# Performance work log

Measured on AMD Instinct MI355X. Metric: run time of the kernel, lower is better.

The kernel has to match this reference:

```python
import jax, jax.numpy as jnp
import numpy as np

TIME_SCALES = [1, 2, 4]
K = len(TIME_SCALES)      # 3 scales
N = 4                     # lcm(time_scales)
S = sum(TIME_SCALES)      # 7 slots
D_HEAD = 128              # d
D = S * D_HEAD            # 896
IO_DIM = 1024
RANK = 64
HIDDEN = 4 * D            # 3584
EPS = 1e-5


def _tables():
    active = np.empty((N, K), dtype=np.int64)
    perm = np.empty((N, K, N), dtype=np.int64)
    inv = np.empty((N, K, N), dtype=np.int64)
    ids = np.arange(N)
    for ph in range(N):
        off = 0
        for k, s in enumerate(TIME_SCALES):
            active[ph, k] = off + ph % s
            off += s
            j = ph % s
            alpha = N // s
            p = (ids + alpha * j) % N   # SHARED assignment
            perm[ph, k] = p
            ip = np.empty_like(p)
            ip[p] = ids
            inv[ph, k] = ip
    return active, perm, inv

ACTIVE, PERM, INV = _tables()


def _ln(x, scale, bias):
    mu = jnp.mean(x, axis=-1, keepdims=True)
    var = jnp.mean((x - mu) ** 2, axis=-1, keepdims=True)
    return (x - mu) * jax.lax.rsqrt(var + EPS) * scale + bias


def setup_inputs() -> dict:
    key = jax.random.key(0)
    ks = jax.random.split(key, 16)
    B, T = 8, 1024

    def w(k, shape, s=0.02):
        return jax.random.normal(k, shape, dtype=jnp.float32) * s

    return {
        "x": jax.random.normal(ks[0], (B, T, IO_DIM), dtype=jnp.float32),
        "enc_base_w": w(ks[1], (D, IO_DIM)),
        "enc_A_w": w(ks[2], (RANK, IO_DIM)),
        "enc_B": w(ks[3], (RANK, N, D)),
        "enc_beta": jnp.float32(0.01),
        "Wqkv": w(ks[4], (K, N, D_HEAD, 3 * D_HEAD)),
        "ln_attn_scale": jnp.ones((D_HEAD,), jnp.float32),
        "ln_attn_bias": jnp.zeros((D_HEAD,), jnp.float32),
        "ln_mixer_scale": jnp.ones((D,), jnp.float32),
        "ln_mixer_bias": jnp.zeros((D,), jnp.float32),
        "mixer_w1": w(ks[5], (HIDDEN, D)),
        "mixer_b1": jnp.zeros((HIDDEN,), jnp.float32),
        "mixer_w2": w(ks[6], (D, HIDDEN)),
        "mixer_b2": jnp.zeros((D,), jnp.float32),
        "dec_ln_scale": jnp.ones((N * D,), jnp.float32),
        "dec_ln_bias": jnp.zeros((N * D,), jnp.float32),
        "dec_down_w": w(ks[7], (RANK, N * D)),
        "dec_up_w": w(ks[8], (IO_DIM, RANK)),
        "phase": 1,
    }


def reference(x, enc_base_w, enc_A_w, enc_B, enc_beta, Wqkv,
              ln_attn_scale, ln_attn_bias, ln_mixer_scale, ln_mixer_bias,
              mixer_w1, mixer_b1, mixer_w2, mixer_b2,
              dec_ln_scale, dec_ln_bias, dec_down_w, dec_up_w, phase):
    B, T, _ = x.shape
    # ---- StreamLoRAEncoder: x [B,T,io] -> z0 [B,T,N,D]
    base = x @ enc_base_w.T                 # [B,T,D]
    h = x @ enc_A_w.T                       # [B,T,r]
    delta = jnp.einsum('btr,rnd->btnd', h, enc_B)
    z0 = base[:, :, None, :] + enc_beta * delta
    # ---- gather active slots for this phase (one slot per scale group)
    slots = ACTIVE[phase]                   # [K]
    z_slots = z0.reshape(B, T, N, S, D_HEAD)
    x_slot = z_slots[:, :, :, slots, :]     # [B,T,N,K,d]
    x_slot = _ln(x_slot, ln_attn_scale, ln_attn_bias)
    # ---- SHARED qkv projection (stream->head inverse perm, bmm, head->stream perm)
    x_in = x_slot.transpose(0, 1, 3, 2, 4)  # [B,T,K,N,d]
    kk = np.arange(K)[:, None]
    x_head = x_in[:, :, kk, INV[phase], :]  # [B,T,K,N,d]
    qkv = jnp.einsum('btknd,knde->btkne', x_head, Wqkv)  # [B,T,K,N,3d]
    qh, kh, vh = jnp.split(qkv, 3, axis=-1)
    p = PERM[phase]
    q = qh[:, :, kk, p, :].transpose(0, 3, 2, 1, 4).reshape(B, N * K, T, D_HEAD)
    k_ = kh[:, :, kk, p, :].transpose(0, 3, 2, 1, 4).reshape(B, N * K, T, D_HEAD)
    v = vh[:, :, kk, p, :].transpose(0, 3, 2, 1, 4).reshape(B, N * K, T, D_HEAD)
    # ---- causal attention over T per (stream, scale) head
    scores = jnp.einsum('bhtd,bhsd->bhts', q, k_) / np.float32(np.sqrt(D_HEAD))
    mask = jnp.tril(jnp.ones((T, T), dtype=bool))
    scores = jnp.where(mask, scores, jnp.float32(-1e9))
    attn = jax.nn.softmax(scores, axis=-1)
    out = jnp.einsum('bhts,bhsd->bhtd', attn, v)  # [B,N*K,T,d]
    # ---- scatter back to active slots (residual add)
    out5 = out.reshape(B, N, K, T, D_HEAD).transpose(0, 3, 1, 2, 4)  # [B,T,N,K,d]
    z1 = z_slots.at[:, :, :, slots, :].add(out5).reshape(B, T, N, D)
    # ---- mixer MLP (pre-LN residual)
    hm = _ln(z1, ln_mixer_scale, ln_mixer_bias)
    m = jax.nn.gelu(hm @ mixer_w1.T + mixer_b1, approximate=False) @ mixer_w2.T + mixer_b2
    z2 = z1 + m
    # ---- StreamLoRADecoder: concat streams, LN, rank-bottleneck projection
    cat = z2.reshape(B, T, N * D)
    y = _ln(cat, dec_ln_scale, dec_ln_bias) @ dec_down_w.T @ dec_up_w.T
    return y
```

## Files before the change

kernel.cpp:

```cpp
#include <hip/hip_runtime.h>
#include <hip/hip_bf16.h>
#include <math.h>


#define BT   8192
#define DH   128
#define DD   896
#define ND   3584
#define IO   1024
#define RK   64
#define HID  3584

typedef __attribute__((ext_vector_type(8))) short short8;
typedef __attribute__((ext_vector_type(4))) float f32x4;
typedef __hip_bfloat16 bf16;

#define DS_READ_B128(dst, p)                                                  \
    asm volatile("ds_read_b128 %0, %1"                                        \
                 : "=v"(dst)                                                  \
                 : "v"((const __attribute__((address_space(3))) bf16*)(p)))

__device__ __forceinline__ float gelu_f(float v)
{
    float u = v * 0.70710678118654752f;
    float a = fabsf(u);
    float t = __builtin_amdgcn_rcpf(1.0f + 0.3275911f * a);
    float p = t * (0.254829592f + t * (-0.284496736f + t * (1.421413741f +
              t * (-1.453152027f + t * 1.061405429f))));
    float er = 1.0f - p * __expf(-u * u);
    er = copysignf(er, u);
    return 0.5f * v * (1.0f + er);
}

template<int BM, int BN, int BK, int TM, int TN>
__global__ __launch_bounds__(256) void gemm_kernel(const float* __restrict__ A,
                                                   const float* __restrict__ B,
                                                   float* __restrict__ C,
                                                   int N, int Kd)
{
    constexpr int THREADS = (BM / TM) * (BN / TN);
    constexpr int LDA = BM + 4;
    constexpr int LDB = BN + 4;
    __shared__ float As[BK][LDA];
    __shared__ float Bs[BK][LDB];

    const int tid = threadIdx.x;
    constexpr int NX = BN / TN;
    const int tx = tid % NX;
    const int ty = tid / NX;
    const int row0 = blockIdx.y * BM;
    const int col0 = blockIdx.x * BN;

    float acc[TM][TN];
#pragma unroll
    for (int i = 0; i < TM; ++i)
#pragma unroll
        for (int j = 0; j < TN; ++j) acc[i][j] = 0.f;

    for (int k0 = 0; k0 < Kd; k0 += BK) {
        constexpr int AF4 = BM * BK / 4;
        for (int f = tid; f < AF4; f += THREADS) {
            int r  = f / (BK / 4);
            int c4 = (f % (BK / 4)) * 4;
            float4 v = *(const float4*)(A + (size_t)(row0 + r) * Kd + k0 + c4);
            As[c4 + 0][r] = v.x; As[c4 + 1][r] = v.y;
            As[c4 + 2][r] = v.z; As[c4 + 3][r] = v.w;
        }
        constexpr int BF4 = BN * BK / 4;
        for (int f = tid; f < BF4; f += THREADS) {
            int r  = f / (BK / 4);
            int c4 = (f % (BK / 4)) * 4;
            float4 v = *(const float4*)(B + (size_t)(col0 + r) * Kd + k0 + c4);
            Bs[c4 + 0][r] = v.x; Bs[c4 + 1][r] = v.y;
            Bs[c4 + 2][r] = v.z; Bs[c4 + 3][r] = v.w;
        }
        __syncthreads();

#pragma unroll
        for (int kk = 0; kk < BK; ++kk) {
            float a[TM], b[TN];
#pragma unroll
            for (int i = 0; i < TM; i += 4)
                *(float4*)&a[i] = *(const float4*)&As[kk][ty * TM + i];
#pragma unroll
            for (int j = 0; j < TN; j += 4)
                *(float4*)&b[j] = *(const float4*)&Bs[kk][tx * TN + j];
#pragma unroll
            for (int i = 0; i < TM; ++i)
#pragma unroll
                for (int j = 0; j < TN; ++j)
                    acc[i][j] = fmaf(a[i], b[j], acc[i][j]);
        }
        __syncthreads();
    }

    const int crow = row0 + ty * TM;
    const int ccol = col0 + tx * TN;
#pragma unroll
    for (int i = 0; i < TM; ++i) {
        float* cp = C + (size_t)(crow + i) * N + ccol;
#pragma unroll
        for (int j = 0; j < TN; ++j) cp[j] = acc[i][j];
    }
}

template<int BN, int EPI>
__global__ __launch_bounds__(512, 2) void gemm_bf16_256(
    const bf16* __restrict__ A,
    const bf16* __restrict__ B,
    float* __restrict__ Cf,
    bf16* __restrict__ Cb,
    int N, int Kd,
    const float* __restrict__ bias)
{
    constexpr int NR    = BN / 64;
    constexpr int WTN   = 16 * NR;
    constexpr int ASLOT = 256 * 32;
    constexpr int BSLOT = BN * 32;
    __shared__ bf16 As[4 * ASLOT];
    __shared__ bf16 Bs[4 * BSLOT];

    const int tid  = threadIdx.x;
    const int wave = tid >> 6;
    const int lane = tid & 63;
    const int wm = wave >> 2, wn = wave & 3;
    const int lr = lane & 15, lq = lane >> 4;

    const int gx  = gridDim.x;
    int fid = blockIdx.y * gx + blockIdx.x;
    const int cpx = (gx * gridDim.y) >> 3;
    fid = (fid & 7) * cpx + (fid >> 3);
    const int row0 = (fid / gx) * 256;
    const int col0 = (fid % gx) * BN;

    const int sr  = lane >> 2;
    const int scs = (((lane & 3) ^ ((lane >> 3) & 3)) << 3);
    const bf16* Ag = A + (size_t)(row0 + sr) * Kd + scs;
    const bf16* Bg = B + (size_t)(col0 + sr) * Kd + scs;

    const int scox = (lq * 8) ^ (((lr >> 1) & 3) << 3);

    f32x4 acc[8][NR];
#pragma unroll
    for (int i = 0; i < 8; ++i)
#pragma unroll
        for (int j = 0; j < NR; ++j) acc[i][j] = (f32x4){0.f, 0.f, 0.f, 0.f};

    const int NH = Kd >> 5;

    auto stage = [&](int h) {
        const int slot = h & 3;
#pragma unroll
        for (int i = 0; i < 2; ++i) {
            const int rg = (i * 8 + wave) * 16;
            __builtin_amdgcn_global_load_lds(
                (const __attribute__((address_space(1))) unsigned int*)
                    (Ag + (size_t)rg * Kd + h * 32),
                (__attribute__((address_space(3))) unsigned int*)
                    (As + slot * ASLOT + rg * 32),
                16, 0, 0);
        }
#pragma unroll
        for (int i = 0; i < BN / 128; ++i) {
            const int rg = (i * 8 + wave) * 16;
            __builtin_amdgcn_global_load_lds(
                (const __attribute__((address_space(1))) unsigned int*)
                    (Bg + (size_t)rg * Kd + h * 32),
                (__attribute__((address_space(3))) unsigned int*)
                    (Bs + slot * BSLOT + rg * 32),
                16, 0, 0);
        }
    };

    stage(0); stage(1); stage(2);

    for (int h = 0; h < NH; ++h) {
        if (h + 3 < NH) stage(h + 3);

        const int ahead = NH - 1 - h;
        if constexpr (BN == 256) {
            if (ahead >= 3)      asm volatile("s_waitcnt vmcnt(12)" ::: "memory");
            else if (ahead == 2) asm volatile("s_waitcnt vmcnt(8)"  ::: "memory");
            else if (ahead == 1) asm volatile("s_waitcnt vmcnt(4)"  ::: "memory");
            else                 asm volatile("s_waitcnt vmcnt(0)"  ::: "memory");
        } else {
            if (ahead >= 3)      asm volatile("s_waitcnt vmcnt(9)"  ::: "memory");
            else if (ahead == 2) asm volatile("s_waitcnt vmcnt(6)"  ::: "memory");
            else if (ahead == 1) asm volatile("s_waitcnt vmcnt(3)"  ::: "memory");
            else                 asm volatile("s_waitcnt vmcnt(0)"  ::: "memory");
        }
        __builtin_amdgcn_s_barrier();

        const bf16* Ab = As + (h & 3) * ASLOT;
        const bf16* Bb = Bs + (h & 3) * BSLOT;

        short8 bfr[NR], afr[8];
#pragma unroll
        for (int nt = 0; nt < NR; ++nt)
            DS_READ_B128(bfr[nt], Bb + (wn * WTN + nt * 16 + lr) * 32 + scox);
#pragma unroll
        for (int mt = 0; mt < 8; ++mt)
            DS_READ_B128(afr[mt], Ab + (wm * 128 + mt * 16 + lr) * 32 + scox);

        asm volatile("s_waitcnt lgkmcnt(0)" ::: "memory");
        __builtin_amdgcn_sched_barrier(0);

        __builtin_amdgcn_s_setprio(1);
#pragma unroll
        for (int mt = 0; mt < 8; ++mt)
#pragma unroll
            for (int nt = 0; nt < NR; ++nt)
                acc[mt][nt] = __builtin_amdgcn_mfma_f32_16x16x32_bf16(
                    afr[mt], bfr[nt], acc[mt][nt], 0, 0, 0);
        __builtin_amdgcn_s_setprio(0);

        __builtin_amdgcn_s_barrier();
    }

#pragma unroll
    for (int mt = 0; mt < 8; ++mt) {
#pragma unroll
        for (int nt = 0; nt < NR; ++nt) {
            const int col = col0 + wn * WTN + nt * 16 + lr;
            const bool cok = (col < N);
            const float bcol = (EPI == 0 || !cok) ? 0.f : bias[col];
#pragma unroll
            for (int r = 0; r < 4; ++r) {
                const int row = row0 + wm * 128 + mt * 16 + lq * 4 + r;
                float v = acc[mt][nt][r] + bcol;
                if (EPI == 1) {
                    if (cok) Cb[(size_t)row * N + col] = __float2bfloat16(gelu_f(v));
                } else if (EPI == 2) {
                    if (cok) Cf[(size_t)row * N + col] += v;
                } else {
                    if (cok) Cf[(size_t)row * N + col] = v;
                }
            }
        }
    }
}

__global__ __launch_bounds__(256) void pack_enc_kernel(const float* __restrict__ baseW,
                                                       const float* __restrict__ Aw,
                                                       const float* __restrict__ Bv,
                                                       const float* __restrict__ betap,
                                                       bf16* __restrict__ outp)
{
    __shared__ float Ps[64][68];
    __shared__ float Qs[64][68];
    const int tid = threadIdx.x;
    const int e0 = blockIdx.y * 64;
    const int k0 = blockIdx.x * 64;

    for (int f = tid; f < 1024; f += 256) {
        int r = f >> 4, c4 = (f & 15) << 2;
        *(float4*)&Ps[r][c4] = *(const float4*)(Bv + (size_t)r * ND + e0 + c4);
        *(float4*)&Qs[r][c4] = *(const float4*)(Aw + (size_t)r * IO + k0 + c4);
    }
    __syncthreads();

    const int tx = tid & 15, ty = tid >> 4;
    float acc[4][4];
#pragma unroll
    for (int i = 0; i < 4; ++i)
#pragma unroll
        for (int j = 0; j < 4; ++j) acc[i][j] = 0.f;

#pragma unroll 8
    for (int r = 0; r < 64; ++r) {
        float a[4], b[4];
        *(float4*)a = *(const float4*)&Ps[r][ty * 4];
        *(float4*)b = *(const float4*)&Qs[r][tx * 4];
#pragma unroll
        for (int i = 0; i < 4; ++i)
#pragma unroll
            for (int j = 0; j < 4; ++j) acc[i][j] = fmaf(a[i], b[j], acc[i][j]);
    }

    const float beta = betap[0];
#pragma unroll
    for (int i = 0; i < 4; ++i) {
        const int e = e0 + ty * 4 + i;
        const int d = e % DD;
#pragma unroll
        for (int j = 0; j < 4; ++j) {
            const int k = k0 + tx * 4 + j;
            float v = baseW[(size_t)d * IO + k] + beta * acc[i][j];
            outp[(size_t)e * IO + k] = __float2bfloat16(v);
        }
    }
}

__global__ __launch_bounds__(256) void qkv_bf16_kernel(
    const bf16* __restrict__ xh,
    const bf16* __restrict__ Wt,
    bf16* __restrict__ Qg,
    bf16* __restrict__ Kg,
    bf16* __restrict__ Vtg,
    const int* __restrict__ phase_p,
    int go)
{
    __shared__ bf16 As[128 * 64];
    __shared__ bf16 Bs[128 * 64];

    const int ph  = phase_p[0] & 3;
    const int zbl = blockIdx.z;
    const int hh  = (go + zbl) % 12;
    const int n   = hh / 3;
    const int k   = hh % 3;
    const int m   = (k == 0) ? n
                  : (k == 1) ? ((n + 2 * (ph & 1)) & 3)
                             : ((n + (ph & 3)) & 3);
    const bf16* A  = xh + (size_t)zbl * (1024 * 128);
    const bf16* Bw = Wt + (size_t)(k * 4 + m) * (384 * 128);

    const int tid  = threadIdx.x;
    const int wave = tid >> 6;
    const int lane = tid & 63;
    const int wm = wave >> 1, wn = wave & 1;
    const int row0 = blockIdx.y * 128;
    const int col0 = blockIdx.x * 128;
    const int lr = lane & 15;
    const int lq = lane >> 4;
    const int srow = lane >> 3;
    const int scol = (lane & 7) * 8;

    f32x4 acc[4][4];
#pragma unroll
    for (int i = 0; i < 4; ++i)
#pragma unroll
        for (int j = 0; j < 4; ++j) acc[i][j] = (f32x4){0.f, 0.f, 0.f, 0.f};

#pragma unroll
    for (int k0 = 0; k0 < 128; k0 += 64) {
#pragma unroll
        for (int j = 0; j < 4; ++j) {
            const int rg = wave * 32 + j * 8;
            __builtin_amdgcn_global_load_lds(
                (const __attribute__((address_space(1))) unsigned int*)
                    (A + (size_t)(row0 + rg + srow) * 128 + k0 + scol),
                (__attribute__((address_space(3))) unsigned int*)(As + rg * 64),
                16, 0, 0);
        }
#pragma unroll
        for (int j = 0; j < 4; ++j) {
            const int rg = wave * 32 + j * 8;
            __builtin_amdgcn_global_load_lds(
                (const __attribute__((address_space(1))) unsigned int*)
                    (Bw + (size_t)(col0 + rg + srow) * 128 + k0 + scol),
                (__attribute__((address_space(3))) unsigned int*)(Bs + rg * 64),
                16, 0, 0);
        }
        __syncthreads();

#pragma unroll
        for (int s = 0; s < 64; s += 32) {
            short8 af[4], bf[4];
#pragma unroll
            for (int mt = 0; mt < 4; ++mt)
                af[mt] = *(const short8*)&As[(wm * 64 + mt * 16 + lr) * 64 + s + lq * 8];
#pragma unroll
            for (int nt = 0; nt < 4; ++nt)
                bf[nt] = *(const short8*)&Bs[(wn * 64 + nt * 16 + lr) * 64 + s + lq * 8];
#pragma unroll
            for (int mt = 0; mt < 4; ++mt)
#pragma unroll
                for (int nt = 0; nt < 4; ++nt)
                    acc[mt][nt] = __builtin_amdgcn_mfma_f32_16x16x32_bf16(
                        af[mt], bf[nt], acc[mt][nt], 0, 0, 0);
        }
        __syncthreads();
    }

    if (col0 < 256) {
        bf16* C = (col0 == 0 ? Qg : Kg) + (size_t)zbl * (1024 * 128);
#pragma unroll
        for (int mt = 0; mt < 4; ++mt)
#pragma unroll
            for (int nt = 0; nt < 4; ++nt) {
                const int col = wn * 64 + nt * 16 + lr;
#pragma unroll
                for (int r = 0; r < 4; ++r) {
                    const int row = row0 + wm * 64 + mt * 16 + lq * 4 + r;
                    C[(size_t)row * 128 + col] = __float2bfloat16(acc[mt][nt][r]);
                }
            }
    } else {
        bf16* Vt = Vtg + (size_t)zbl * (128 * 1024);
#pragma unroll
        for (int mt = 0; mt < 4; ++mt)
#pragma unroll
            for (int nt = 0; nt < 4; ++nt) {
                const int d = wn * 64 + nt * 16 + lr;
                const int rowb = row0 + wm * 64 + mt * 16 + lq * 4;
                union { bf16 h[4]; uint2 u; } pk;
#pragma unroll
                for (int r = 0; r < 4; ++r)
                    pk.h[r] = __float2bfloat16(acc[mt][nt][r]);
                *(uint2*)(Vt + (size_t)d * 1024 + rowb) = pk.u;
            }
    }
}

__global__ __launch_bounds__(512, 2) void flash_bf16_kernel(
    const bf16* __restrict__ Qg,
    const bf16* __restrict__ Kg,
    const bf16* __restrict__ Vtg,
    float* __restrict__ z,
    const int* __restrict__ phase_p,
    int go, int GQ, int* __restrict__ cnt)
{
    __shared__ bf16 Ks[2 * 64 * 128];
    __shared__ bf16 Vs[128 * 64];
    __shared__ bf16 Ps[128 * 64];
    __shared__ int sw;

    const int ph   = phase_p[0] & 3;
    const int tid  = threadIdx.x;
    const int wave = tid >> 6;
    const int lane = tid & 63;
    const int lr = lane & 15;
    const int lq = lane >> 4;
    const int sr4 = lane >> 4, sc4 = (lane & 15) * 8;
    const int sr8 = lane >> 3, sc8 = (lane & 7) * 8;
    const int swz = (lr & 7) << 3;
    const float sc = 0.08838834764831845f;
    const int nitems = GQ * 8;

    for (;;) {
        __syncthreads();
        if (tid == 0) sw = atomicAdd(cnt, 1);
        __syncthreads();
        const int w = sw;
        if (w >= nitems) return;

        const int wq  = w / GQ;
        const int qy8 = 7 - wq;
        const int zbl = w - wq * GQ;
        const int zb  = go + zbl;
        const int b   = zb / 12;
        const int hh  = zb % 12;
        const int n   = hh / 3;
        const int ksl = hh % 3;
        const int slot = (ksl == 0) ? 0 : (ksl == 1 ? 1 + (ph & 1) : 3 + (ph & 3));
        const int q0  = qy8 * 128;
        const int NT  = qy8 * 2 + 2;

        const bf16* Qp = Qg  + (size_t)zbl * (1024 * 128);
        const bf16* Kp = Kg  + (size_t)zbl * (1024 * 128);
        const bf16* Vp = Vtg + (size_t)zbl * (128 * 1024);

        auto stageK = [&](int t) {
            const int j0 = t * 64;
            bf16* Kd = Ks + (t & 1) * (64 * 128);
#pragma unroll
            for (int j = 0; j < 2; ++j) {
                const int rg = wave * 8 + j * 4;
                const int krow = rg + sr4;
                const int kcol = sc4 ^ ((krow & 7) << 3);
                __builtin_amdgcn_global_load_lds(
                    (const __attribute__((address_space(1))) unsigned int*)
                        (Kp + (size_t)(j0 + krow) * 128 + kcol),
                    (__attribute__((address_space(3))) unsigned int*)(Kd + rg * 128),
                    16, 0, 0);
            }
        };
        auto stageV = [&](int t) {
            const int j0 = t * 64;
#pragma unroll
            for (int j = 0; j < 2; ++j) {
                const int rg = wave * 16 + j * 8;
                const int vrow = rg + sr8;
                const int vcol = sc8 ^ ((vrow & 7) << 3);
                __builtin_amdgcn_global_load_lds(
                    (const __attribute__((address_space(1))) unsigned int*)
                        (Vp + (size_t)vrow * 1024 + j0 + vcol),
                    (__attribute__((address_space(3))) unsigned int*)(Vs + rg * 64),
                    16, 0, 0);
            }
        };

        short8 qreg[4];
#pragma unroll
        for (int s = 0; s < 4; ++s)
            qreg[s] = *(const short8*)(Qp + (size_t)(q0 + wave * 16 + lr) * 128
                                       + s * 32 + lq * 8);

        f32x4 accO[8];
        float m_i[4], l_i[4];
#pragma unroll
        for (int j = 0; j < 8; ++j) accO[j] = (f32x4){0.f, 0.f, 0.f, 0.f};
#pragma unroll
        for (int r = 0; r < 4; ++r) { m_i[r] = -1e30f; l_i[r] = 0.f; }

        stageK(0);

        for (int t = 0; t < NT; ++t) {
            const bool more = (t + 1 < NT);
            if (more) stageK(t + 1);
            stageV(t);
            if (more) asm volatile("s_waitcnt vmcnt(4)" ::: "memory");
            else      asm volatile("s_waitcnt vmcnt(2)" ::: "memory");
            __builtin_amdgcn_s_barrier();
            __builtin_amdgcn_sched_barrier(0);

            const bf16* Kbb = Ks + (t & 1) * (64 * 128);
            const int j0 = t * 64;
            const bool active = (j0 <= q0 + wave * 16 + 15);

            if (active) {
                f32x4 accS[4];
#pragma unroll
                for (int nt = 0; nt < 4; ++nt) accS[nt] = (f32x4){0.f, 0.f, 0.f, 0.f};
                short8 bk[2][4];
#pragma unroll
                for (int nt = 0; nt < 4; ++nt)
                    DS_READ_B128(bk[0][nt],
                                 Kbb + (nt * 16 + lr) * 128 + ((lq * 8) ^ swz));
#pragma unroll
                for (int s = 0; s < 4; ++s) {
                    if (s + 1 < 4) {
#pragma unroll
                        for (int nt = 0; nt < 4; ++nt)
                            DS_READ_B128(bk[(s + 1) & 1][nt],
                                         Kbb + (nt * 16 + lr) * 128
                                             + (((s + 1) * 32 + lq * 8) ^ swz));
                        asm volatile("s_waitcnt lgkmcnt(4)" ::: "memory");
                    } else {
                        asm volatile("s_waitcnt lgkmcnt(0)" ::: "memory");
                    }
                    __builtin_amdgcn_sched_barrier(0);
#pragma unroll
                    for (int nt = 0; nt < 4; ++nt)
                        accS[nt] = __builtin_amdgcn_mfma_f32_16x16x32_bf16(
                            qreg[s], bk[s & 1][nt], accS[nt], 0, 0, 0);
                }

                const bool need_mask = (j0 + 63 > q0 + wave * 16);
#pragma unroll
                for (int r = 0; r < 4; ++r) {
                    const int row = q0 + wave * 16 + lq * 4 + r;
                    float sv[4];
#pragma unroll
                    for (int nt = 0; nt < 4; ++nt) {
                        float v = accS[nt][r] * sc;
                        if (need_mask && (j0 + nt * 16 + lr > row)) v = -1e30f;
                        sv[nt] = v;
                    }
                    float mx = fmaxf(fmaxf(sv[0], sv[1]), fmaxf(sv[2], sv[3]));
#pragma unroll
                    for (int msk = 8; msk; msk >>= 1) mx = fmaxf(mx, __shfl_xor(mx, msk, 16));
                    float mnew = fmaxf(m_i[r], mx);
                    float al   = __expf(m_i[r] - mnew);
                    float rs = 0.f;
#pragma unroll
                    for (int nt = 0; nt < 4; ++nt) {
                        sv[nt] = __expf(sv[nt] - mnew);
                        rs += sv[nt];
                    }
#pragma unroll
                    for (int msk = 8; msk; msk >>= 1) rs += __shfl_xor(rs, msk, 16);
                    l_i[r] = l_i[r] * al + rs;
                    m_i[r] = mnew;
#pragma unroll
                    for (int d8 = 0; d8 < 8; ++d8) accO[d8][r] *= al;
                    const int prow = wave * 16 + lq * 4 + r;
                    const int pswz = (prow & 7) << 3;
#pragma unroll
                    for (int nt = 0; nt < 4; ++nt)
                        Ps[prow * 64 + ((nt * 16 + lr) ^ pswz)] = __float2bfloat16(sv[nt]);
                }
                asm volatile("" ::: "memory");
            }

            if (more) asm volatile("s_waitcnt vmcnt(2)" ::: "memory");
            else      asm volatile("s_waitcnt vmcnt(0)" ::: "memory");
            __builtin_amdgcn_s_barrier();
            __builtin_amdgcn_sched_barrier(0);

            if (active) {
                short8 ap[2], bv[2][8];
                DS_READ_B128(ap[0], Ps + (wave * 16 + lr) * 64 + ((lq * 8) ^ swz));
#pragma unroll
                for (int d8 = 0; d8 < 8; ++d8)
                    DS_READ_B128(bv[0][d8],
                                 Vs + (d8 * 16 + lr) * 64 + ((lq * 8) ^ swz));
#pragma unroll
                for (int kv = 0; kv < 2; ++kv) {
                    if (kv == 0) {
                        DS_READ_B128(ap[1],
                                     Ps + (wave * 16 + lr) * 64 + ((32 + lq * 8) ^ swz));
#pragma unroll
                        for (int d8 = 0; d8 < 8; ++d8)
                            DS_READ_B128(bv[1][d8],
                                         Vs + (d8 * 16 + lr) * 64 + ((32 + lq * 8) ^ swz));
                        asm volatile("s_waitcnt lgkmcnt(9)" ::: "memory");
                    } else {
                        asm volatile("s_waitcnt lgkmcnt(0)" ::: "memory");
                    }
                    __builtin_amdgcn_sched_barrier(0);
#pragma unroll
                    for (int d8 = 0; d8 < 8; ++d8)
                        accO[d8] = __builtin_amdgcn_mfma_f32_16x16x32_bf16(
                            ap[kv], bv[kv][d8], accO[d8], 0, 0, 0);
                }
            }

            __builtin_amdgcn_s_barrier();
        }

#pragma unroll
        for (int r = 0; r < 4; ++r) {
            const int t = q0 + wave * 16 + lq * 4 + r;
            const float inv = 1.0f / l_i[r];
            float* dst = z + (size_t)(b * 1024 + t) * ND + n * DD + slot * DH;
#pragma unroll
            for (int d8 = 0; d8 < 8; ++d8)
                dst[d8 * 16 + lr] += accO[d8][r] * inv;
        }
    }
}

__global__ __launch_bounds__(256) void cvt_bf16_kernel(const float* __restrict__ src,
                                                       bf16* __restrict__ dst,
                                                       int n4)
{
    int i = blockIdx.x * 256 + threadIdx.x;
    if (i < n4) {
        float4 v = ((const float4*)src)[i];
        bf16* d = dst + (size_t)i * 4;
        d[0] = __float2bfloat16(v.x);
        d[1] = __float2bfloat16(v.y);
        d[2] = __float2bfloat16(v.z);
        d[3] = __float2bfloat16(v.w);
    }
}

__global__ __launch_bounds__(256) void cvt_wqkv_kernel(const float* __restrict__ W,
                                                       bf16* __restrict__ Wt)
{
    int o = blockIdx.x * 256 + threadIdx.x;
    if (o < 12 * 384 * 128) {
        int i = o / 49152, rem = o % 49152;
        int e = rem / 128, d = rem % 128;
        Wt[o] = __float2bfloat16(W[(size_t)i * 49152 + d * 384 + e]);
    }
}

__global__ __launch_bounds__(256) void ln_attn_kernel(const float* __restrict__ z,
                                                      bf16* __restrict__ xh,
                                                      const float* __restrict__ scale,
                                                      const float* __restrict__ bias,
                                                      const int* __restrict__ phase_p,
                                                      int bt0)
{
    const int ph   = phase_p[0] & 3;
    const int lane = threadIdx.x & 63;
    const int row  = blockIdx.x * 4 + (threadIdx.x >> 6);
    const int k    = row % 3;
    const int n    = (row / 3) & 3;
    const int btl  = row / 12;
    const int slot = (k == 0) ? 0 : (k == 1 ? 1 + (ph & 1) : 3 + (ph & 3));
    const int bt   = bt0 + btl;

    const float* src = z + (size_t)bt * ND + n * DD + slot * DH + lane * 2;
    float2 v = *(const float2*)src;
    float s = v.x + v.y;
    float q = v.x * v.x + v.y * v.y;
#pragma unroll
    for (int m = 32; m; m >>= 1) { s += __shfl_xor(s, m); q += __shfl_xor(q, m); }
    float mu  = s * (1.0f / 128.0f);
    float var = q * (1.0f / 128.0f) - mu * mu;
    float r   = rsqrtf(var + 1e-5f);

    float2 sc2 = *(const float2*)(scale + lane * 2);
    float2 bi2 = *(const float2*)(bias + lane * 2);
    const int bl = btl >> 10, t = btl & 1023;
    union { bf16 h[2]; unsigned int u; } pk;
    pk.h[0] = __float2bfloat16((v.x - mu) * r * sc2.x + bi2.x);
    pk.h[1] = __float2bfloat16((v.y - mu) * r * sc2.y + bi2.y);
    *(unsigned int*)(xh + (size_t)((bl * 12 + n * 3 + k) * 1024 + t) * DH + lane * 2) = pk.u;
}

template<int W>
__global__ __launch_bounds__(256) void ln_row_bf16_kernel(const float* __restrict__ in,
                                                          bf16* __restrict__ outp,
                                                          const float* __restrict__ scale,
                                                          const float* __restrict__ bias)
{
    constexpr int NIT = (W + 255) / 256;
    const int row = blockIdx.x;
    const int tid = threadIdx.x;
    const float* rp = in + (size_t)row * W;

    float v[NIT];
    float s = 0.f, q = 0.f;
#pragma unroll
    for (int i = 0; i < NIT; ++i) {
        int idx = tid + i * 256;
        if (idx < W) { float t = rp[idx]; v[i] = t; s += t; q += t * t; }
        else v[i] = 0.f;
    }
#pragma unroll
    for (int m = 32; m; m >>= 1) { s += __shfl_xor(s, m); q += __shfl_xor(q, m); }
    __shared__ float ss[4], sq[4];
    if ((tid & 63) == 0) { ss[tid >> 6] = s; sq[tid >> 6] = q; }
    __syncthreads();
    s = ss[0] + ss[1] + ss[2] + ss[3];
    q = sq[0] + sq[1] + sq[2] + sq[3];
    float mu  = s * (1.0f / W);
    float var = q * (1.0f / W) - mu * mu;
    float r   = rsqrtf(var + 1e-5f);

    bf16* op = outp + (size_t)row * W;
#pragma unroll
    for (int i = 0; i < NIT; ++i) {
        int idx = tid + i * 256;
        if (idx < W)
            op[idx] = __float2bfloat16((v[i] - mu) * r * scale[idx] + bias[idx]);
    }
}

extern "C" void kernel_launch(void* const* d_in, const int* in_sizes, int n_in,
                              void* d_out, int out_size, void* d_ws, size_t ws_size,
                              hipStream_t stream)
{
    const float* x          = (const float*)d_in[0];
    const float* enc_base_w = (const float*)d_in[1];
    const float* enc_A_w    = (const float*)d_in[2];
    const float* enc_B      = (const float*)d_in[3];
    const float* enc_beta   = (const float*)d_in[4];
    const float* Wqkv       = (const float*)d_in[5];
    const float* ln_attn_s  = (const float*)d_in[6];
    const float* ln_attn_b  = (const float*)d_in[7];
    const float* ln_mix_s   = (const float*)d_in[8];
    const float* ln_mix_b   = (const float*)d_in[9];
    const float* w1         = (const float*)d_in[10];
    const float* b1         = (const float*)d_in[11];
    const float* w2         = (const float*)d_in[12];
    const float* b2         = (const float*)d_in[13];
    const float* dec_ln_s   = (const float*)d_in[14];
    const float* dec_ln_b   = (const float*)d_in[15];
    const float* dec_down   = (const float*)d_in[16];
    const float* dec_up     = (const float*)d_in[17];
    const int*   phase_p    = (const int*)d_in[18];
    float* out = (float*)d_out;

    float* ws = (float*)d_ws;
    float* z  = ws;
    float* R  = ws + (size_t)BT * ND;

    const int GQ = (ws_size >= 230000000UL) ? 96 : 48;
    const int CH = (ws_size >= 205000000UL) ? 8192 : 4096;

    bf16* xb   = (bf16*)R;
    bf16* Wenc = xb + (size_t)BT * IO;
    bf16* Wt   = (bf16*)R;
    bf16* xh_b = Wt + 12 * 384 * 128;
    bf16* Qb   = xh_b + (size_t)GQ * 1024 * 128;
    bf16* Kb   = Qb + (size_t)GQ * 1024 * 128;
    bf16* Vtg  = Kb + (size_t)GQ * 1024 * 128;
    int*  cnt  = (int*)(Vtg + (size_t)GQ * 128 * 1024);
    bf16* w1b  = (bf16*)R;
    bf16* w2b  = w1b + (size_t)HID * DD;
    bf16* hm   = w2b + (size_t)DD * HID;
    bf16* gbuf = hm + (size_t)CH * DD;
    bf16*  zb  = (bf16*)R;
    bf16*  ddp = zb + (size_t)BT * ND;
    float* t1  = (float*)(ddp + 128 * ND);

    cvt_bf16_kernel<<<dim3(8192), 256, 0, stream>>>(x, xb, BT * IO / 4);
    pack_enc_kernel<<<dim3(16, 56), 256, 0, stream>>>(enc_base_w, enc_A_w, enc_B,
                                                      enc_beta, Wenc);
    gemm_bf16_256<256, 0><<<dim3(14, 32), 512, 0, stream>>>(xb, Wenc, z, nullptr,
                                                            ND, IO, nullptr);

    cvt_wqkv_kernel<<<dim3(2304), 256, 0, stream>>>(Wqkv, Wt);
    hipMemsetAsync(cnt, 0, 2 * sizeof(int), stream);
    const int ngroups = 96 / GQ;
    for (int g = 0; g < ngroups; ++g) {
        ln_attn_kernel<<<dim3(GQ * 256), 256, 0, stream>>>(z, xh_b, ln_attn_s,
                                                           ln_attn_b, phase_p,
                                                           g * (GQ / 12) * 1024);
        qkv_bf16_kernel<<<dim3(3, 8, GQ), 256, 0, stream>>>(xh_b, Wt, Qb, Kb, Vtg,
                                                            phase_p, g * GQ);
        flash_bf16_kernel<<<dim3(512), 512, 0, stream>>>(Qb, Kb, Vtg, z,
                                                         phase_p, g * GQ, GQ,
                                                         cnt + g);
    }

    cvt_bf16_kernel<<<dim3(3136), 256, 0, stream>>>(w1, w1b, HID * DD / 4);
    cvt_bf16_kernel<<<dim3(3136), 256, 0, stream>>>(w2, w2b, DD * HID / 4);
    for (int c = 0; c < 32768 / CH; ++c) {
        float* zc = z + (size_t)c * CH * DD;
        ln_row_bf16_kernel<896><<<dim3(CH), 256, 0, stream>>>(zc, hm,
                                                              ln_mix_s, ln_mix_b);
        gemm_bf16_256<256, 1><<<dim3(14, CH / 256), 512, 0, stream>>>(
            hm, w1b, nullptr, gbuf, HID, DD, b1);
        gemm_bf16_256<128, 2><<<dim3(7, CH / 256), 512, 0, stream>>>(
            gbuf, w2b, zc, nullptr, DD, HID, b2);
    }

    ln_row_bf16_kernel<3584><<<dim3(8192), 256, 0, stream>>>(z, zb,
                                                             dec_ln_s, dec_ln_b);
    hipMemsetAsync(ddp + (size_t)64 * ND, 0, (size_t)64 * ND * sizeof(bf16),
                   stream);
    cvt_bf16_kernel<<<dim3(224), 256, 0, stream>>>(dec_down, ddp, 64 * ND / 4);
    gemm_bf16_256<128, 0><<<dim3(1, 32), 512, 0, stream>>>(zb, ddp, t1, nullptr,
                                                           RK, ND, nullptr);
    gemm_kernel<128, 128, 16, 8, 8>
        <<<dim3(8, 64), 256, 0, stream>>>(t1, dec_up, out, IO, RK);
}
```

Measured before the change: 1.226 ms.

## Split-K decoder GEMM, static flash work pairing, split LDS wait in GEMM

The decoder down-projection GEMM previously ran on only 32 blocks. It is now split along K into 8 slices, and each slice atomically adds its result into a zeroed fp32 buffer. The flash attention kernel drops its atomic work-queue counter. Instead it uses a static grid of GQ*5 blocks that pairs long and short causal query tiles (7, 6+0, 5+1, 4+2, 3) to balance the work. The GEMM main loop now starts MFMAs on the first half of the A fragments before the remaining LDS reads finish, which risks float atomic nondeterminism and a memset cost.

Measured after the change: 1.184 ms. 1.04x faster.

```diff
diff --git a/kernel.cpp b/kernel.cpp
--- a/kernel.cpp
+++ b/kernel.cpp
@@ -133,10 +133,13 @@
     const int row0 = (fid / gx) * 256;
     const int col0 = (fid % gx) * BN;
 
+    const int klen = Kd / (int)gridDim.z;
+    const int kbeg = blockIdx.z * klen;
+
     const int sr  = lane >> 2;
     const int scs = (((lane & 3) ^ ((lane >> 3) & 3)) << 3);
-    const bf16* Ag = A + (size_t)(row0 + sr) * Kd + scs;
-    const bf16* Bg = B + (size_t)(col0 + sr) * Kd + scs;
+    const bf16* Ag = A + (size_t)(row0 + sr) * Kd + kbeg + scs;
+    const bf16* Bg = B + (size_t)(col0 + sr) * Kd + kbeg + scs;
 
     const int scox = (lq * 8) ^ (((lr >> 1) & 3) << 3);
 
@@ -146,7 +149,7 @@
 #pragma unroll
         for (int j = 0; j < NR; ++j) acc[i][j] = (f32x4){0.f, 0.f, 0.f, 0.f};
 
-    const int NH = Kd >> 5;
+    const int NH = klen >> 5;
 
     auto stage = [&](int h) {
         const int slot = h & 3;
@@ -202,18 +205,30 @@
         for (int mt = 0; mt < 8; ++mt)
             DS_READ_B128(afr[mt], Ab + (wm * 128 + mt * 16 + lr) * 32 + scox);
 
-        asm volatile("s_waitcnt lgkmcnt(0)" ::: "memory");
+        asm volatile("s_waitcnt lgkmcnt(4)" ::: "memory");
         __builtin_amdgcn_sched_barrier(0);
 
         __builtin_amdgcn_s_setprio(1);
 #pragma unroll
-        for (int mt = 0; mt < 8; ++mt)
+        for (int mt = 0; mt < 4; ++mt)
 #pragma unroll
             for (int nt = 0; nt < NR; ++nt)
                 acc[mt][nt] = __builtin_amdgcn_mfma_f32_16x16x32_bf16(
                     afr[mt], bfr[nt], acc[mt][nt], 0, 0, 0);
         __builtin_amdgcn_s_setprio(0);
 
+        asm volatile("s_waitcnt lgkmcnt(0)" ::: "memory");
+        __builtin_amdgcn_sched_barrier(0);
+
+        __builtin_amdgcn_s_setprio(1);
+#pragma unroll
+        for (int mt = 4; mt < 8; ++mt)
+#pragma unroll
+            for (int nt = 0; nt < NR; ++nt)
+                acc[mt][nt] = __builtin_amdgcn_mfma_f32_16x16x32_bf16(
+                    afr[mt], bfr[nt], acc[mt][nt], 0, 0, 0);
+        __builtin_amdgcn_s_setprio(0);
+
         __builtin_amdgcn_s_barrier();
     }
 
@@ -223,7 +238,7 @@
         for (int nt = 0; nt < NR; ++nt) {
             const int col = col0 + wn * WTN + nt * 16 + lr;
             const bool cok = (col < N);
-            const float bcol = (EPI == 0 || !cok) ? 0.f : bias[col];
+            const float bcol = (EPI == 0 || EPI == 3 || !cok) ? 0.f : bias[col];
 #pragma unroll
             for (int r = 0; r < 4; ++r) {
                 const int row = row0 + wm * 128 + mt * 16 + lq * 4 + r;
@@ -232,6 +247,8 @@
                     if (cok) Cb[(size_t)row * N + col] = __float2bfloat16(gelu_f(v));
                 } else if (EPI == 2) {
                     if (cok) Cf[(size_t)row * N + col] += v;
+                } else if (EPI == 3) {
+                    if (cok) atomicAdd(Cf + (size_t)row * N + col, v);
                 } else {
                     if (cok) Cf[(size_t)row * N + col] = v;
                 }
@@ -408,12 +425,11 @@
     const bf16* __restrict__ Vtg,
     float* __restrict__ z,
     const int* __restrict__ phase_p,
-    int go, int GQ, int* __restrict__ cnt)
+    int go, int GQ)
 {
     __shared__ bf16 Ks[2 * 64 * 128];
     __shared__ bf16 Vs[128 * 64];
     __shared__ bf16 Ps[128 * 64];
-    __shared__ int sw;
 
     const int ph   = phase_p[0] & 3;
     const int tid  = threadIdx.x;
@@ -425,60 +441,58 @@
     const int sr8 = lane >> 3, sc8 = (lane & 7) * 8;
     const int swz = (lr & 7) << 3;
     const float sc = 0.08838834764831845f;
-    const int nitems = GQ * 8;
-
-    for (;;) {
-        __syncthreads();
-        if (tid == 0) sw = atomicAdd(cnt, 1);
-        __syncthreads();
-        const int w = sw;
-        if (w >= nitems) return;
-
-        const int wq  = w / GQ;
-        const int qy8 = 7 - wq;
-        const int zbl = w - wq * GQ;
-        const int zb  = go + zbl;
-        const int b   = zb / 12;
-        const int hh  = zb % 12;
-        const int n   = hh / 3;
-        const int ksl = hh % 3;
-        const int slot = (ksl == 0) ? 0 : (ksl == 1 ? 1 + (ph & 1) : 3 + (ph & 3));
+
+    const int zbl = blockIdx.x % GQ;
+    const int grp = blockIdx.x / GQ;
+    const int zb  = go + zbl;
+    const int b   = zb / 12;
+    const int hh  = zb % 12;
+    const int n   = hh / 3;
+    const int ksl = hh % 3;
+    const int slot = (ksl == 0) ? 0 : (ksl == 1 ? 1 + (ph & 1) : 3 + (ph & 3));
+
+    const bf16* Qp = Qg  + (size_t)zbl * (1024 * 128);
+    const bf16* Kp = Kg  + (size_t)zbl * (1024 * 128);
+    const bf16* Vp = Vtg + (size_t)zbl * (128 * 1024);
+
+    auto stageK = [&](int t) {
+        const int j0 = t * 64;
+        bf16* Kd = Ks + (t & 1) * (64 * 128);
+#pragma unroll
+        for (int j = 0; j < 2; ++j) {
+            const int rg = wave * 8 + j * 4;
+            const int krow = rg + sr4;
+            const int kcol = sc4 ^ ((krow & 7) << 3);
+            __builtin_amdgcn_global_load_lds(
+                (const __attribute__((address_space(1))) unsigned int*)
+                    (Kp + (size_t)(j0 + krow) * 128 + kcol),
+                (__attribute__((address_space(3))) unsigned int*)(Kd + rg * 128),
+                16, 0, 0);
+        }
+    };
+    auto stageV = [&](int t) {
+        const int j0 = t * 64;
+#pragma unroll
+        for (int j = 0; j < 2; ++j) {
+            const int rg = wave * 16 + j * 8;
+            const int vrow = rg + sr8;
+            const int vcol = sc8 ^ ((vrow & 7) << 3);
+            __builtin_amdgcn_global_load_lds(
+                (const __attribute__((address_space(1))) unsigned int*)
+                    (Vp + (size_t)vrow * 1024 + j0 + vcol),
+                (__attribute__((address_space(3))) unsigned int*)(Vs + rg * 64),
+                16, 0, 0);
+        }
+    };
+
+    const int qa_t[5] = {7, 6, 5, 4, 3};
+    const int qb_t[5] = {-1, 0, 1, 2, -1};
+
+    for (int part = 0; part < 2; ++part) {
+        const int qy8 = (part == 0) ? qa_t[grp] : qb_t[grp];
+        if (qy8 < 0) break;
         const int q0  = qy8 * 128;
         const int NT  = qy8 * 2 + 2;
-
-        const bf16* Qp = Qg  + (size_t)zbl * (1024 * 128);
-        const bf16* Kp = Kg  + (size_t)zbl * (1024 * 128);
-        const bf16* Vp = Vtg + (size_t)zbl * (128 * 1024);
-
-        auto stageK = [&](int t) {
-            const int j0 = t * 64;
-            bf16* Kd = Ks + (t & 1) * (64 * 128);
-#pragma unroll
-            for (int j = 0; j < 2; ++j) {
-                const int rg = wave * 8 + j * 4;
-                const int krow = rg + sr4;
-                const int kcol = sc4 ^ ((krow & 7) << 3);
-                __builtin_amdgcn_global_load_lds(
-                    (const __attribute__((address_space(1))) unsigned int*)
-                        (Kp + (size_t)(j0 + krow) * 128 + kcol),
-                    (__attribute__((address_space(3))) unsigned int*)(Kd + rg * 128),
-                    16, 0, 0);
-            }
-        };
-        auto stageV = [&](int t) {
-            const int j0 = t * 64;
-#pragma unroll
-            for (int j = 0; j < 2; ++j) {
-                const int rg = wave * 16 + j * 8;
-                const int vrow = rg + sr8;
-                const int vcol = sc8 ^ ((vrow & 7) << 3);
-                __builtin_amdgcn_global_load_lds(
-                    (const __attribute__((address_space(1))) unsigned int*)
-                        (Vp + (size_t)vrow * 1024 + j0 + vcol),
-                    (__attribute__((address_space(3))) unsigned int*)(Vs + rg * 64),
-                    16, 0, 0);
-            }
-        };
 
         short8 qreg[4];
 #pragma unroll
@@ -760,7 +774,6 @@
     bf16* Qb   = xh_b + (size_t)GQ * 1024 * 128;
     bf16* Kb   = Qb + (size_t)GQ * 1024 * 128;
     bf16* Vtg  = Kb + (size_t)GQ * 1024 * 128;
-    int*  cnt  = (int*)(Vtg + (size_t)GQ * 128 * 1024);
     bf16* w1b  = (bf16*)R;
     bf16* w2b  = w1b + (size_t)HID * DD;
     bf16* hm   = w2b + (size_t)DD * HID;
@@ -776,7 +789,6 @@
                                                             ND, IO, nullptr);
 
     cvt_wqkv_kernel<<<dim3(2304), 256, 0, stream>>>(Wqkv, Wt);
-    hipMemsetAsync(cnt, 0, 2 * sizeof(int), stream);
     const int ngroups = 96 / GQ;
     for (int g = 0; g < ngroups; ++g) {
         ln_attn_kernel<<<dim3(GQ * 256), 256, 0, stream>>>(z, xh_b, ln_attn_s,
@@ -784,9 +796,8 @@
                                                            g * (GQ / 12) * 1024);
         qkv_bf16_kernel<<<dim3(3, 8, GQ), 256, 0, stream>>>(xh_b, Wt, Qb, Kb, Vtg,
                                                             phase_p, g * GQ);
-        flash_bf16_kernel<<<dim3(512), 512, 0, stream>>>(Qb, Kb, Vtg, z,
-                                                         phase_p, g * GQ, GQ,
-                                                         cnt + g);
+        flash_bf16_kernel<<<dim3(GQ * 5), 512, 0, stream>>>(Qb, Kb, Vtg, z,
+                                                            phase_p, g * GQ, GQ);
     }
 
     cvt_bf16_kernel<<<dim3(3136), 256, 0, stream>>>(w1, w1b, HID * DD / 4);
@@ -806,8 +817,10 @@
     hipMemsetAsync(ddp + (size_t)64 * ND, 0, (size_t)64 * ND * sizeof(bf16),
                    stream);
     cvt_bf16_kernel<<<dim3(224), 256, 0, stream>>>(dec_down, ddp, 64 * ND / 4);
-    gemm_bf16_256<128, 0><<<dim3(1, 32), 512, 0, stream>>>(zb, ddp, t1, nullptr,
-                                                           RK, ND, nullptr);
+    hipMemsetAsync(t1, 0, (size_t)BT * RK * sizeof(float), stream);
+    gemm_bf16_256<128, 3><<<dim3(1, 32, 8), 512, 0, stream>>>(zb, ddp, t1,
+                                                              nullptr, RK, ND,
+                                                              nullptr);
     gemm_kernel<128, 128, 16, 8, 8>
         <<<dim3(8, 64), 256, 0, stream>>>(t1, dec_up, out, IO, RK);
 }
```
